# Performance work log

Hardware: AMD Instinct MI355X
Metric: run time of the kernel (lower is better)

Reference implementation:

```python
import jax, jax.numpy as jnp
import numpy as np

B, T, C = 48, 200, 53          # batch, timepoints, ICA components
E, H, A = 32, 64, 64            # embed dim, GRU hidden dim, attention hidden dim
C2 = C * C                      # 2809
E1 = round(0.05 * C2)           # gta_embed out = 140
E2 = round(0.5 * C2)            # gta_attend hidden = 1404
O = 2                           # output classes
BN_EPS = 1e-5


def setup_inputs() -> dict:
    key = jax.random.key(0)
    ks = jax.random.split(key, 24)
    n = lambda k, shape, s: jax.random.normal(k, shape, dtype=jnp.float32) * s
    return {
        "x": jax.random.normal(ks[0], (B, T, C), dtype=jnp.float32),
        "emb_w": n(ks[1], (E,), 0.3), "emb_b": n(ks[2], (E,), 0.1),
        "w_ih": n(ks[3], (3 * H, E), 0.12), "w_hh": n(ks[4], (3 * H, H), 0.12),
        "b_ih": n(ks[5], (3 * H,), 0.05), "b_hh": n(ks[6], (3 * H,), 0.05),
        "wq": n(ks[7], (A, H), 0.12), "bq": n(ks[8], (A,), 0.05),
        "wk": n(ks[9], (A, H), 0.12), "bk": n(ks[10], (A,), 0.05),
        "wv": n(ks[11], (H, H), 0.12), "bv": n(ks[12], (H,), 0.05),
        "u0": jax.random.normal(ks[13], (H,), dtype=jnp.float32),
        "w_g1": n(ks[14], (E1, C2), 0.02), "b_g1": n(ks[15], (E1,), 0.02),
        "bn_g": jnp.ones((E1,), jnp.float32), "bn_b": jnp.zeros((E1,), jnp.float32),
        "w_g2": n(ks[16], (E2, E1), 0.05), "b_g2": n(ks[17], (E2,), 0.05),
        "w_g3": n(ks[18], (1, E2), 0.02), "b_g3": n(ks[19], (1,), 0.02),
        "w_clf": n(ks[20], (O, C2), 0.02), "b_clf": jnp.zeros((O,), jnp.float32),
    }


def _normalize(v, eps=1e-12):
    return v / (jnp.linalg.norm(v) + eps)


def _gru_cell(x, h, w_ih, w_hh, b_ih, b_hh):
    # torch GRU cell math. x:(N,E) h:(N,H)
    gi = x @ w_ih.T + b_ih
    gh = h @ w_hh.T + b_hh
    i_r, i_z, i_n = jnp.split(gi, 3, axis=-1)
    h_r, h_z, h_n = jnp.split(gh, 3, axis=-1)
    r = jax.nn.sigmoid(i_r + h_r)
    z = jax.nn.sigmoid(i_z + h_z)
    n = jnp.tanh(i_n + r * h_n)
    return (1.0 - z) * n + z * h


def _forward(x, emb_w, emb_b, w_ih, w_hh, b_ih, b_hh, wq, bq, wk, bk, wv, bv, u0,
             w_g1, b_g1, bn_g, bn_b, w_g2, b_g2, w_g3, b_g3, w_clf, b_clf):
    Bs, Ts, Cs = x.shape
    Hd = wv.shape[0]
    # single shared Linear(1,E) embedding: (B,T,C) -> (T,B,C,E) for scan
    emb = x[..., None] * emb_w + emb_b
    emb = jnp.transpose(emb, (1, 0, 2, 3))
    h0 = jnp.zeros((Bs * Cs, Hd), x.dtype)

    def step(carry, emb_t):
        h, u = carry
        hg = _gru_cell(emb_t.reshape(Bs * Cs, -1), h, w_ih, w_hh, b_ih, b_hh)
        hb = hg.reshape(Bs, Cs, Hd)
        # spectral_norm on value weight: 5 power iterations (no_grad, as torch)
        v = None
        for _ in range(5):
            v = _normalize(wv.T @ u)
            u = _normalize(wv @ v)
        u = jax.lax.stop_gradient(u)
        v = jax.lax.stop_gradient(v)
        sigma = u @ (wv @ v)
        q = hb @ wq.T + bq          # (B,C,A)
        k = hb @ wk.T + bk          # (B,C,A)
        val = hb @ (wv / sigma).T + bv  # (B,C,H)
        scores = jnp.einsum('bia,bja->bij', q, k)  # (B,C,C)
        # eigenvalue-based spectral normalization (detached: track_grads=False)
        ev = jnp.linalg.eigvals(jax.lax.stop_gradient(scores))
        m = jnp.max(jnp.abs(ev), axis=1)[:, None, None].astype(x.dtype)
        attn = scores / m
        h_new = jnp.einsum('bij,bjh->bih', attn, val).reshape(Bs * Cs, Hd)
        return (h_new, u), attn

    (_, _), aligns = jax.lax.scan(step, (h0, u0), emb)  # aligns: (T,B,C,C)
    align = jnp.transpose(aligns, (1, 0, 2, 3))         # (B,T,C,C)
    Aflat = align.reshape(Bs, Ts, Cs * Cs)

    # gta_attention over the time axis
    xr = Aflat * Aflat.mean(axis=1, keepdims=True)
    flat = xr.reshape(Bs * Ts, Cs * Cs)
    e = flat @ w_g1.T + b_g1
    mu = e.mean(axis=0)
    var = e.var(axis=0)  # biased, as torch BatchNorm1d (training)
    e = jax.nn.relu((e - mu) / jnp.sqrt(var + BN_EPS) * bn_g + bn_b)
    a = jax.nn.relu(e @ w_g2.T + b_g2) @ w_g3.T + b_g3   # (B*T,1)
    a = jax.nn.softmax(a.reshape(Bs, Ts), axis=1)
    dnc = (Aflat * a[..., None]).sum(axis=1)             # (B,C*C)
    logits = dnc @ w_clf.T + b_clf
    return logits, dnc.reshape(Bs, Cs, Cs), align


def reference(x, emb_w, emb_b, w_ih, w_hh, b_ih, b_hh, wq, bq, wk, bk, wv, bv, u0,
              w_g1, b_g1, bn_g, bn_b, w_g2, b_g2, w_g3, b_g3, w_clf, b_clf):
    return _forward(x, emb_w, emb_b, w_ih, w_hh, b_ih, b_hh, wq, bq, wk, bk, wv, bv, u0,
                    w_g1, b_g1, bn_g, bn_b, w_g2, b_g2, w_g3, b_g3, w_clf, b_clf)
```

## Files before the change

kernel.cpp:

```cpp
#include <hip/hip_runtime.h>
#include <hip/hip_bf16.h>
#include <math.h>

#define B_  48
#define T_  200
#define C_  53
#define H_  64
#define C2_ 2809
#define E1_ 140
#define E2_ 1404
#define TS  60

typedef long long i64;

struct __align__(16) F4 { float v[4]; };

__device__ __forceinline__ float wredsum(float v){
  #pragma unroll
  for (int o = 32; o > 0; o >>= 1) v += __shfl_xor(v, o);
  return v;
}
__device__ __forceinline__ float sigm(float x){ return 1.f/(1.f + __expf(-x)); }
__device__ __forceinline__ float tanhx(float x){
  float a = fabsf(x);
  float e = __expf(-2.f*a);
  float t = (1.f - e)/(1.f + e);
  return copysignf(t, x);
}

__device__ __forceinline__ void eig_mm(const float* __restrict__ X, float* __restrict__ Y,
                                       int r0, int c0, float inv,
                                       float& essq, float& etrc){
  float ea0[4] = {0.f,0.f,0.f,0.f};
  float ea1[4] = {0.f,0.f,0.f,0.f};
  for (int kq = 0; kq < 13; kq++){
    int k4 = kq*4;
    F4 a0 = *(const F4*)&X[(r0+0)*TS + k4];
    F4 a1 = *(const F4*)&X[(r0+1)*TS + k4];
    F4 b0 = *(const F4*)&X[(k4+0)*TS + c0];
    F4 b1 = *(const F4*)&X[(k4+1)*TS + c0];
    F4 b2 = *(const F4*)&X[(k4+2)*TS + c0];
    F4 b3 = *(const F4*)&X[(k4+3)*TS + c0];
    #pragma unroll
    for (int ci = 0; ci < 4; ci++){
      ea0[ci] += a0.v[0]*b0.v[ci] + a0.v[1]*b1.v[ci] + a0.v[2]*b2.v[ci] + a0.v[3]*b3.v[ci];
      ea1[ci] += a1.v[0]*b0.v[ci] + a1.v[1]*b1.v[ci] + a1.v[2]*b2.v[ci] + a1.v[3]*b3.v[ci];
    }
  }
  {
    float a0 = X[(r0+0)*TS + 52], a1 = X[(r0+1)*TS + 52];
    F4 bb = *(const F4*)&X[52*TS + c0];
    #pragma unroll
    for (int ci = 0; ci < 4; ci++){ ea0[ci] += a0*bb.v[ci]; ea1[ci] += a1*bb.v[ci]; }
  }
  F4 o0, o1;
  #pragma unroll
  for (int ci = 0; ci < 4; ci++){
    o0.v[ci] = ea0[ci]*inv;
    o1.v[ci] = ea1[ci]*inv;
    essq += o0.v[ci]*o0.v[ci] + o1.v[ci]*o1.v[ci];
  }
  if (r0   >= c0 && r0   < c0+4) etrc += o0.v[r0-c0];
  if (r0+1 >= c0 && r0+1 < c0+4) etrc += o1.v[r0+1-c0];
  *(F4*)&Y[(r0+0)*TS + c0] = o0;
  *(F4*)&Y[(r0+1)*TS + c0] = o1;
}

#define OFF_SIGMA 0
#define OFF_WHHT  200
#define OFF_WZV   12488
#define OFF_WUV   20680
#define OFF_P     20812
#define OFF_R0    21004
#define OFF_MM    21196
#define OFF_M2    25292
#define OFF_M4    29388
#define OFF_M5    33484
#define OFF_AMEAN 37580
#define OFF_E     172412
#define OFF_CA    1516412
#define OFF_CB    1516552
#define OFF_APRE  1516692
#define OFF_A     1526292
#define OFF_G2T   1535892

__global__ void k_prep1(const float* __restrict__ w_hh, const float* __restrict__ wq,
                        const float* __restrict__ wk, const float* __restrict__ wv,
                        const float* __restrict__ w_ih, const float* __restrict__ emb_w,
                        const float* __restrict__ emb_b, const float* __restrict__ b_ih,
                        const float* __restrict__ bq, const float* __restrict__ bk,
                        const float* __restrict__ w_g2,
                        float* whhT, float* wzv, float* wuv, float* g2t,
                        float* p, float* r0){
  int idx0 = blockIdx.x*blockDim.x + threadIdx.x;
  int stride = gridDim.x*blockDim.x;
  for (int i = idx0; i < 64*192; i += stride){
    int kk = i/192, g = i%192;
    whhT[i] = w_hh[g*64 + kk];
  }
  for (int i = idx0; i < 8192; i += stride){
    int h = i >> 7, a = i & 127;
    if (a < 64){
      float g = 0.f;
      for (int m = 0; m < 64; m++) g += wq[m*64 + h]*wk[m*64 + a];
      wzv[i] = g;
    } else {
      wzv[i] = wv[(a-64)*64 + h];
    }
  }
  for (int i = idx0; i < 129; i += stride){
    if (i < 64){
      float s = 0.f;
      for (int m = 0; m < 64; m++) s += wq[m*64 + i]*bk[m];
      wuv[i] = s;
    } else if (i < 128){
      int h = i - 64;
      float s = 0.f;
      for (int m = 0; m < 64; m++) s += wk[m*64 + h]*bq[m];
      wuv[i] = s;
    } else {
      float s = 0.f;
      for (int m = 0; m < 64; m++) s += bq[m]*bk[m];
      wuv[128] = s;
    }
  }
  for (int i = idx0; i < 140*1404; i += stride){ int k = i/1404, n = i%1404; g2t[i] = w_g2[n*140+k]; }
  for (int i = idx0; i < 192; i += stride){
    float s1 = 0.f, s2 = 0.f;
    for (int e = 0; e < 32; e++){ float w = w_ih[i*32+e]; s1 += w*emb_w[e]; s2 += w*emb_b[e]; }
    p[i] = s1; r0[i] = s2 + b_ih[i];
  }
}

__global__ void k_prep2(const float* __restrict__ wv, const float* __restrict__ u0,
                        float* Wm, float* Wm2, float* Wm4, float* Wm5, float* sigma){
  int r = threadIdx.x;
  for (int c = 0; c < 64; c++){
    float s = 0.f;
    for (int k = 0; k < 64; k++) s += wv[r*64+k]*wv[c*64+k];
    Wm[r*64+c] = s;
  }
  __syncthreads();
  for (int c = 0; c < 64; c++){
    float s = 0.f;
    for (int k = 0; k < 64; k++) s += Wm[r*64+k]*Wm[k*64+c];
    Wm2[r*64+c] = s;
  }
  __syncthreads();
  for (int c = 0; c < 64; c++){
    float s = 0.f;
    for (int k = 0; k < 64; k++) s += Wm2[r*64+k]*Wm2[k*64+c];
    Wm4[r*64+c] = s;
  }
  __syncthreads();
  for (int c = 0; c < 64; c++){
    float s = 0.f;
    for (int k = 0; k < 64; k++) s += Wm4[r*64+k]*Wm[k*64+c];
    Wm5[r*64+c] = s;
  }
  __syncthreads();
  __shared__ float su[64];
  su[r] = u0[r];
  __syncthreads();
  for (int t = 0; t < T_; t++){
    float z = 0.f, w = 0.f;
    for (int k = 0; k < 64; k++){ float uk = su[k]; z += Wm4[r*64+k]*uk; w += Wm5[r*64+k]*uk; }
    float nw = wredsum(w*w);
    float zw = wredsum(z*w);
    float sg = sqrtf(nw / fmaxf(zw, 1e-35f));
    if (r == 0) sigma[t] = sg;
    float wn = w * (1.f/sqrtf(fmaxf(nw, 1e-35f)));
    __syncthreads();
    su[r] = wn;
    __syncthreads();
  }
}

__global__ __launch_bounds__(512, 1) void k_scan(
    const float* __restrict__ x, const float* __restrict__ b_hh,
    const float* __restrict__ bv,
    const float* __restrict__ whhT, const float* __restrict__ wzv,
    const float* __restrict__ wuv,
    const float* __restrict__ wp, const float* __restrict__ wr0,
    const float* __restrict__ sigma, float* __restrict__ outAL,
    float* __restrict__ wamean){
  __shared__ __align__(16) float L[34160];
  float* Lw  = L;
  float* Rh  = L + 12288;
  float* R4  = L + 16128;
  float* R3  = L + 19968;
  float* R2  = L + 23808;
  float* R1  = L + 27200;
  float* Lp  = L + 30560;
  float* Lr0 = L + 30752;
  float* Lbh = L + 30944;
  float* Lbv = L + 31136;
  float* Lrq = L + 31200;
  float* Lrk = L + 31256;
  float* Lsc = L + 31312;
  float* Lmean = L + 31344;
  int tid = threadIdx.x;
  int b = blockIdx.x;

  for (int i = tid; i < 3072; i += 512) *(F4*)&Lw[i*4] = *(const F4*)&whhT[i*4];
  for (int i = tid; i < 192; i += 512){ Lp[i] = wp[i]; Lr0[i] = wr0[i]; Lbh[i] = b_hh[i]; }
  for (int i = tid; i < 64; i += 512) Lbv[i] = bv[i];
  for (int i = tid; i < 18272; i += 512) L[12288 + i] = 0.f;
  for (int i = tid; i < 2816; i += 512) Lmean[i] = 0.f;
  __syncthreads();

  int ct4 = tid >> 4, jt4 = tid & 15;
  int c0g = ct4*4, j0g = jt4*4;
  int it14 = tid/14, jt14 = tid%14;
  int i0s = it14*4, j0s = jt14*4;
  int ctq = tid >> 5, gtq = tid & 31;
  int c0q = ctq*4, g0q = gtq*4;
  int erg = tid/14, ecg = tid%14;
  int er0 = erg*2, ec0 = ecg*4;

  const float c0v = wuv[128];

  for (int t = 0; t < T_; t++){
    if (tid < 32) Lsc[tid] = 0.f;
    if (tid < 224){
      float gacc[3][4][4];
      #pragma unroll
      for (int g = 0; g < 3; g++)
        #pragma unroll
        for (int ji = 0; ji < 4; ji++){
          float bb = Lbh[g*64 + j0g + ji];
          #pragma unroll
          for (int ci = 0; ci < 4; ci++) gacc[g][ji][ci] = bb;
        }
      for (int kk = 0; kk < 64; kk++){
        F4 hv = *(F4*)&Rh[kk*TS + c0g];
        F4 w0 = *(const F4*)&Lw[kk*192 + j0g];
        F4 w1 = *(const F4*)&Lw[kk*192 + 64 + j0g];
        F4 w2 = *(const F4*)&Lw[kk*192 + 128 + j0g];
        #pragma unroll
        for (int ji = 0; ji < 4; ji++)
          #pragma unroll
          for (int ci = 0; ci < 4; ci++){
            gacc[0][ji][ci] += hv.v[ci]*w0.v[ji];
            gacc[1][ji][ci] += hv.v[ci]*w1.v[ji];
            gacc[2][ji][ci] += hv.v[ci]*w2.v[ji];
          }
      }
      float xv[4];
      #pragma unroll
      for (int ci = 0; ci < 4; ci++){
        int c = c0g + ci;
        xv[ci] = (c < C_) ? x[(i64)(b*T_ + t)*C_ + c] : 0.f;
      }
      F4 p0 = *(F4*)&Lp[j0g], p1 = *(F4*)&Lp[64+j0g], p2 = *(F4*)&Lp[128+j0g];
      F4 q0 = *(F4*)&Lr0[j0g], q1 = *(F4*)&Lr0[64+j0g], q2 = *(F4*)&Lr0[128+j0g];
      #pragma unroll
      for (int ji = 0; ji < 4; ji++){
        F4 hold = *(F4*)&Rh[(j0g+ji)*TS + c0g];
        F4 o;
        #pragma unroll
        for (int ci = 0; ci < 4; ci++){
          float rr = sigm(xv[ci]*p0.v[ji] + q0.v[ji] + gacc[0][ji][ci]);
          float zz = sigm(xv[ci]*p1.v[ji] + q1.v[ji] + gacc[1][ji][ci]);
          float nn = tanhx(xv[ci]*p2.v[ji] + q2.v[ji] + rr*gacc[2][ji][ci]);
          float hg = (1.f - zz)*nn + zz*hold.v[ci];
          o.v[ci] = (c0g + ci < C_) ? hg : 0.f;
        }
        *(F4*)&R4[(j0g+ji)*TS + c0g] = o;
      }
    }
    __syncthreads();
    if (tid < 448){
      float acc[4][4];
      #pragma unroll
      for (int gi = 0; gi < 4; gi++)
        #pragma unroll
        for (int ci = 0; ci < 4; ci++) acc[gi][ci] = 0.f;
      for (int kk = 0; kk < 64; kk++){
        F4 a = *(F4*)&R4[kk*TS + c0q];
        F4 w = *(const F4*)&wzv[kk*128 + g0q];
        #pragma unroll
        for (int gi = 0; gi < 4; gi++)
          #pragma unroll
          for (int ci = 0; ci < 4; ci++) acc[gi][ci] += a.v[ci]*w.v[gi];
      }
      if (g0q < 64){
        #pragma unroll
        for (int gi = 0; gi < 4; gi++){
          F4 o;
          #pragma unroll
          for (int ci = 0; ci < 4; ci++) o.v[ci] = acc[gi][ci];
          *(F4*)&R3[(g0q+gi)*TS + c0q] = o;
        }
      } else {
        float invs = 1.f/sigma[t];
        int a0i = g0q - 64;
        #pragma unroll
        for (int ci = 0; ci < 4; ci++){
          int c = c0q + ci;
          if (c < C_){
            F4 o;
            #pragma unroll
            for (int gi = 0; gi < 4; gi++) o.v[gi] = acc[gi][ci]*invs + Lbv[a0i+gi];
            *(F4*)&R2[c*64 + a0i] = o;
          }
        }
      }
    } else if (tid < 504){
      int u = tid - 448;
      float rq = 0.f, rk = 0.f;
      if (u < C_){
        for (int h = 0; h < 64; h++){
          float hv = R4[h*TS + u];
          rq += hv*wuv[h];
          rk += hv*wuv[64+h];
        }
      }
      if (u < 56){ Lrq[u] = rq; Lrk[u] = rk; }
    }
    __syncthreads();
    {
      float sacc[4][4];
      float ssq = 0.f, trc = 0.f;
      if (tid < 196){
        #pragma unroll
        for (int ii = 0; ii < 4; ii++)
          #pragma unroll
          for (int jj = 0; jj < 4; jj++){
            int i = i0s + ii, j = j0s + jj;
            sacc[ii][jj] = (i < C_ && j < C_) ? (Lrq[i] + Lrk[j] + c0v) : 0.f;
          }
        for (int aq = 0; aq < 16; aq++){
          int a4 = aq*4;
          F4 qa0 = *(F4*)&R3[(a4+0)*TS + i0s];
          F4 qa1 = *(F4*)&R3[(a4+1)*TS + i0s];
          F4 qa2 = *(F4*)&R3[(a4+2)*TS + i0s];
          F4 qa3 = *(F4*)&R3[(a4+3)*TS + i0s];
          F4 kb0 = *(F4*)&R4[(a4+0)*TS + j0s];
          F4 kb1 = *(F4*)&R4[(a4+1)*TS + j0s];
          F4 kb2 = *(F4*)&R4[(a4+2)*TS + j0s];
          F4 kb3 = *(F4*)&R4[(a4+3)*TS + j0s];
          #pragma unroll
          for (int ii = 0; ii < 4; ii++)
            #pragma unroll
            for (int jj = 0; jj < 4; jj++)
              sacc[ii][jj] += qa0.v[ii]*kb0.v[jj] + qa1.v[ii]*kb1.v[jj]
                            + qa2.v[ii]*kb2.v[jj] + qa3.v[ii]*kb3.v[jj];
        }
        #pragma unroll
        for (int ii = 0; ii < 4; ii++){
          int i = i0s + ii;
          if (i < C_){
            F4 o;
            #pragma unroll
            for (int jj = 0; jj < 4; jj++){
              o.v[jj] = sacc[ii][jj];
              ssq += sacc[ii][jj]*sacc[ii][jj];
            }
            *(F4*)&R1[i*TS + j0s] = o;
            if (j0s <= i && i < j0s + 4) trc += sacc[ii][i - j0s];
          }
        }
      }
      ssq = wredsum(ssq); trc = wredsum(trc);
      if ((tid & 63) == 0){
        if (ssq != 0.f) atomicAdd(&Lsc[0], ssq);
        if (trc != 0.f) atomicAdd(&Lsc[1], trc);
      }
    }
    __syncthreads();
    {
      float inv0 = 1.f/fmaxf(Lsc[0], 1e-35f);
      float essq = 0.f, etrc = 0.f;
      if (tid < 378) eig_mm(R1, R3, er0, ec0, inv0, essq, etrc);
      essq = wredsum(essq); etrc = wredsum(etrc);
      if ((tid & 63) == 0){
        if (essq != 0.f) atomicAdd(&Lsc[2], essq);
        if (etrc != 0.f) atomicAdd(&Lsc[3], etrc);
      }
    }
    __syncthreads();
    float Gacc = 0.f, prevest = 1e30f, est = 0.f;
    int cnt = 0;
    float pssq = fmaxf(Lsc[0], 1e-35f), ptr1 = Lsc[1];
    float* Xb = R3; float* Yb = R4;
    for (int j = 2; j <= 13; j++){
      float sj = fmaxf(Lsc[2*(j-1)], 1e-35f);
      float tj = Lsc[2*(j-1)+1];
      int J = j - 2;
      float t1n = ptr1/sqrtf(pssq);
      float t2n = tj;
      float disc = 2.f*t2n - t1n*t1n;
      float rq = (disc >= 0.f) ? 0.5f*(fabsf(t1n) + sqrtf(disc))
                               : sqrtf(fmaxf(0.5f*(t1n*t1n - t2n), 1e-30f));
      rq = fminf(fmaxf(rq, 0.02f), 1.5f);
      est = Gacc + ldexpf(0.5f*log2f(pssq) + log2f(rq), -J);
      if (fabsf(est - prevest) < 1e-4f) cnt++; else cnt = 0;
      prevest = est;
      Gacc += ldexpf(log2f(pssq), -(J+1));
      if ((J >= 4 && cnt >= 1) || j == 13) break;
      pssq = sj; ptr1 = tj;
      {
        float inv = 1.f/sj;
        float essq = 0.f, etrc = 0.f;
        if (tid < 378) eig_mm(Xb, Yb, er0, ec0, inv, essq, etrc);
        essq = wredsum(essq); etrc = wredsum(etrc);
        if ((tid & 63) == 0){
          if (essq != 0.f) atomicAdd(&Lsc[2*j], essq);
          if (etrc != 0.f) atomicAdd(&Lsc[2*j+1], etrc);
        }
      }
      { float* tp = Xb; Xb = Yb; Yb = tp; }
      __syncthreads();
    }
    float invm = exp2f(-est);
    if (tid < 224){
      float hraw0[4] = {0.f,0.f,0.f,0.f};
      float hraw1[4] = {0.f,0.f,0.f,0.f};
      float hraw2[4] = {0.f,0.f,0.f,0.f};
      float hraw3[4] = {0.f,0.f,0.f,0.f};
      for (int kq = 0; kq < 13; kq++){
        int k4 = kq*4;
        F4 a0 = *(F4*)&R1[(c0g+0)*TS + k4];
        F4 a1 = *(F4*)&R1[(c0g+1)*TS + k4];
        F4 a2 = *(F4*)&R1[(c0g+2)*TS + k4];
        F4 a3 = *(F4*)&R1[(c0g+3)*TS + k4];
        F4 b0 = *(F4*)&R2[(k4+0)*64 + j0g];
        F4 b1 = *(F4*)&R2[(k4+1)*64 + j0g];
        F4 b2 = *(F4*)&R2[(k4+2)*64 + j0g];
        F4 b3 = *(F4*)&R2[(k4+3)*64 + j0g];
        #pragma unroll
        for (int jj = 0; jj < 4; jj++){
          hraw0[jj] += a0.v[0]*b0.v[jj] + a0.v[1]*b1.v[jj] + a0.v[2]*b2.v[jj] + a0.v[3]*b3.v[jj];
          hraw1[jj] += a1.v[0]*b0.v[jj] + a1.v[1]*b1.v[jj] + a1.v[2]*b2.v[jj] + a1.v[3]*b3.v[jj];
          hraw2[jj] += a2.v[0]*b0.v[jj] + a2.v[1]*b1.v[jj] + a2.v[2]*b2.v[jj] + a2.v[3]*b3.v[jj];
          hraw3[jj] += a3.v[0]*b0.v[jj] + a3.v[1]*b1.v[jj] + a3.v[2]*b2.v[jj] + a3.v[3]*b3.v[jj];
        }
      }
      {
        const int k = 52;
        float a0 = R1[(c0g+0)*TS + k], a1 = R1[(c0g+1)*TS + k];
        float a2 = R1[(c0g+2)*TS + k], a3 = R1[(c0g+3)*TS + k];
        F4 bb = *(F4*)&R2[k*64 + j0g];
        #pragma unroll
        for (int jj = 0; jj < 4; jj++){
          hraw0[jj] += a0*bb.v[jj];
          hraw1[jj] += a1*bb.v[jj];
          hraw2[jj] += a2*bb.v[jj];
          hraw3[jj] += a3*bb.v[jj];
        }
      }
      #pragma unroll
      for (int jj = 0; jj < 4; jj++){
        F4 o;
        o.v[0] = (c0g + 0 < C_) ? hraw0[jj]*invm : 0.f;
        o.v[1] = (c0g + 1 < C_) ? hraw1[jj]*invm : 0.f;
        o.v[2] = (c0g + 2 < C_) ? hraw2[jj]*invm : 0.f;
        o.v[3] = (c0g + 3 < C_) ? hraw3[jj]*invm : 0.f;
        *(F4*)&Rh[(j0g+jj)*TS + c0g] = o;
      }
    } else if (tid < 420){
      int u = tid - 224;
      int i0 = (u/14)*4, j0 = (u%14)*4;
      float* ALrow = outAL + (i64)(b*T_ + t)*C2_;
      #pragma unroll
      for (int ii = 0; ii < 4; ii++){
        int i = i0 + ii;
        if (i < C_){
          F4 s = *(F4*)&R1[i*TS + j0];
          #pragma unroll
          for (int jj = 0; jj < 4; jj++){
            int jc = j0 + jj;
            if (jc < C_){
              float v = s.v[jj]*invm;
              ALrow[i*C_ + jc] = v;
              Lmean[i*C_ + jc] += v;
            }
          }
        }
      }
    }
    __syncthreads();
  }
  for (int i = tid; i < C2_; i += 512)
    wamean[(i64)b*C2_ + i] = Lmean[i]*(1.f/(float)T_);
}

__global__ __launch_bounds__(128) void k_gemm1(const float* __restrict__ AL,
                                               const float* __restrict__ amean,
                                               const float* __restrict__ w_g1,
                                               float* __restrict__ e){
  __shared__ __align__(16) float At[64][68];
  __shared__ __align__(16) float Bt[64][148];
  int mt = blockIdx.x >> 2, ks = blockIdx.x & 3;
  int tid = threadIdx.x;
  float acc[8][12];
  #pragma unroll
  for (int ri = 0; ri < 8; ri++)
    #pragma unroll
    for (int ci = 0; ci < 12; ci++) acc[ri][ci] = 0.f;
  int rg = tid/12, cg = tid%12;
  int r0 = rg*8, cc0 = cg*12;
  for (int kb = 0; kb < 11; kb++){
    int k0 = (ks*11 + kb)*64;
    for (int idx = tid; idx < 4096; idx += 128){
      int r = idx >> 6, i = idx & 63;
      int kk = k0 + i;
      int row = mt*64 + r, bb = row/T_;
      float v = 0.f;
      if (kk < C2_) v = AL[(i64)row*C2_ + kk]*amean[(i64)bb*C2_ + kk];
      At[i][r] = v;
    }
    for (int idx = tid; idx < 9216; idx += 128){
      int c = idx >> 6, i = idx & 63;
      int kk = k0 + i;
      float v = 0.f;
      if (c < E1_ && kk < C2_) v = w_g1[(i64)c*C2_ + kk];
      Bt[i][c] = v;
    }
    __syncthreads();
    if (tid < 96){
      for (int i = 0; i < 64; i++){
        F4 a0 = *(F4*)&At[i][r0]; F4 a1 = *(F4*)&At[i][r0+4];
        F4 b0 = *(F4*)&Bt[i][cc0]; F4 b1 = *(F4*)&Bt[i][cc0+4]; F4 b2 = *(F4*)&Bt[i][cc0+8];
        #pragma unroll
        for (int ri = 0; ri < 8; ri++){
          float av = (ri < 4) ? a0.v[ri] : a1.v[ri-4];
          #pragma unroll
          for (int ci = 0; ci < 12; ci++){
            float bv = (ci < 4) ? b0.v[ci] : (ci < 8) ? b1.v[ci-4] : b2.v[ci-8];
            acc[ri][ci] += av*bv;
          }
        }
      }
    }
    __syncthreads();
  }
  if (tid < 96){
    #pragma unroll
    for (int ri = 0; ri < 8; ri++)
      #pragma unroll
      for (int ci = 0; ci < 12; ci++){
        int c = cc0 + ci;
        if (c < E1_) atomicAdd(&e[(i64)(mt*64 + r0 + ri)*E1_ + c], acc[ri][ci]);
      }
  }
}

__global__ void k_bnstats(const float* __restrict__ e, const float* __restrict__ bn_g,
                          const float* __restrict__ bn_b, float* cA, float* cB){
  __shared__ float s1a[256], s2a[256];
  int c = blockIdx.x, tid = threadIdx.x;
  float s1 = 0.f, s2 = 0.f;
  for (int row = tid; row < B_*T_; row += 256){
    float v = e[(i64)row*E1_ + c];
    s1 += v; s2 += v*v;
  }
  s1a[tid] = s1; s2a[tid] = s2; __syncthreads();
  for (int s = 128; s > 0; s >>= 1){
    if (tid < s){ s1a[tid] += s1a[tid+s]; s2a[tid] += s2a[tid+s]; }
    __syncthreads();
  }
  if (tid == 0){
    float n = (float)(B_*T_);
    float mu = s1a[0]/n;
    float var = s2a[0]/n - mu*mu;
    float a = bn_g[c]/sqrtf(var + 1e-5f);
    cA[c] = a; cB[c] = bn_b[c] - mu*a;
  }
}

__global__ __launch_bounds__(128) void k_gemm2(const float* __restrict__ e,
                                               const float* __restrict__ cA, const float* __restrict__ cB,
                                               const float* __restrict__ g2t,
                                               const float* __restrict__ b_g2, const float* __restrict__ w_g3,
                                               float* __restrict__ apre){
  __shared__ __align__(16) float At2[140][68];
  int mt = blockIdx.x/30, nc = blockIdx.x%30;
  int tid = threadIdx.x;
  int nbase = nc*48;
  for (int idx = tid; idx < 64*140; idx += 128){
    int r = idx/140, k = idx - r*140;
    float v = e[(i64)(mt*64 + r)*E1_ + k]*cA[k] + cB[k];
    At2[k][r] = fmaxf(v, 0.f);
  }
  __syncthreads();
  if (tid < 96){
    int rg = tid/6, ng = tid%6;
    int r0 = rg*4, n0 = nbase + ng*8;
    float acc[4][8];
    #pragma unroll
    for (int ri = 0; ri < 4; ri++)
      #pragma unroll
      for (int ni = 0; ni < 8; ni++) acc[ri][ni] = 0.f;
    for (int k = 0; k < E1_; k++){
      F4 a = *(F4*)&At2[k][r0];
      float bvv[8];
      if (n0 + 8 <= E2_){
        F4 b0 = *(const F4*)&g2t[(i64)k*E2_ + n0];
        F4 b1 = *(const F4*)&g2t[(i64)k*E2_ + n0 + 4];
        #pragma unroll
        for (int u = 0; u < 4; u++){ bvv[u] = b0.v[u]; bvv[u+4] = b1.v[u]; }
      } else {
        #pragma unroll
        for (int ni = 0; ni < 8; ni++){ int n = n0+ni; bvv[ni] = (n < E2_) ? g2t[(i64)k*E2_ + n] : 0.f; }
      }
      #pragma unroll
      for (int ri = 0; ri < 4; ri++)
        #pragma unroll
        for (int ni = 0; ni < 8; ni++) acc[ri][ni] += a.v[ri]*bvv[ni];
    }
    #pragma unroll
    for (int ri = 0; ri < 4; ri++){
      float s = 0.f;
      #pragma unroll
      for (int ni = 0; ni < 8; ni++){
        int n = n0 + ni;
        if (n < E2_){
          float a2 = acc[ri][ni] + b_g2[n];
          if (a2 > 0.f) s += a2*w_g3[n];
        }
      }
      atomicAdd(&apre[mt*64 + r0 + ri], s);
    }
  }
}

__global__ void k_soft(const float* __restrict__ apre, const float* __restrict__ b_clf,
                       float* __restrict__ wa, float* __restrict__ out){
  __shared__ float sr[256];
  int b = blockIdx.x, tid = threadIdx.x;
  float v = (tid < T_) ? apre[b*T_ + tid] : -3.4e38f;
  sr[tid] = v; __syncthreads();
  for (int s = 128; s > 0; s >>= 1){ if (tid < s) sr[tid] = fmaxf(sr[tid], sr[tid+s]); __syncthreads(); }
  float mx = sr[0]; __syncthreads();
  float ev = (tid < T_) ? __expf(v - mx) : 0.f;
  sr[tid] = ev; __syncthreads();
  for (int s = 128; s > 0; s >>= 1){ if (tid < s) sr[tid] += sr[tid+s]; __syncthreads(); }
  float den = sr[0];
  if (tid < T_) wa[b*T_ + tid] = ev/den;
  if (b == 0 && tid < 2*B_) out[tid] = b_clf[tid & 1];
}

__global__ void k_dnc(const float* __restrict__ AL, const float* __restrict__ wa,
                      const float* __restrict__ w_clf, float* __restrict__ out){
  int b = blockIdx.x/11, ch = blockIdx.x%11;
  int c2 = ch*256 + threadIdx.x;
  float acc = 0.f;
  if (c2 < C2_){
    for (int t = 0; t < T_; t++)
      acc += AL[(i64)(b*T_ + t)*C2_ + c2]*wa[b*T_ + t];
    out[96 + (i64)b*C2_ + c2] = acc;
  }
  float p0 = (c2 < C2_) ? acc*w_clf[c2]        : 0.f;
  float p1 = (c2 < C2_) ? acc*w_clf[C2_ + c2]  : 0.f;
  p0 = wredsum(p0); p1 = wredsum(p1);
  if ((threadIdx.x & 63) == 0){
    atomicAdd(&out[b*2 + 0], p0);
    atomicAdd(&out[b*2 + 1], p1);
  }
}

extern "C" void kernel_launch(void* const* d_in, const int* in_sizes, int n_in,
                              void* d_out, int out_size, void* d_ws, size_t ws_size,
                              hipStream_t stream){
  const float* x     = (const float*)d_in[0];
  const float* emb_w = (const float*)d_in[1];
  const float* emb_b = (const float*)d_in[2];
  const float* w_ih  = (const float*)d_in[3];
  const float* w_hh  = (const float*)d_in[4];
  const float* b_ih  = (const float*)d_in[5];
  const float* b_hh  = (const float*)d_in[6];
  const float* wq    = (const float*)d_in[7];
  const float* bq    = (const float*)d_in[8];
  const float* wk    = (const float*)d_in[9];
  const float* bk    = (const float*)d_in[10];
  const float* wv_in = (const float*)d_in[11];
  const float* bv    = (const float*)d_in[12];
  const float* u0    = (const float*)d_in[13];
  const float* w_g1  = (const float*)d_in[14];
  const float* bn_g  = (const float*)d_in[16];
  const float* bn_b  = (const float*)d_in[17];
  const float* w_g2  = (const float*)d_in[18];
  const float* b_g2  = (const float*)d_in[19];
  const float* w_g3  = (const float*)d_in[20];
  const float* w_clf = (const float*)d_in[22];
  const float* b_clf = (const float*)d_in[23];
  float* out = (float*)d_out;
  float* W = (float*)d_ws;

  float* wsig   = W + OFF_SIGMA;
  float* whhT   = W + OFF_WHHT;
  float* wzv    = W + OFF_WZV;
  float* wuv    = W + OFF_WUV;
  float* wp     = W + OFF_P;
  float* wr0    = W + OFF_R0;
  float* wM     = W + OFF_MM;
  float* wM2    = W + OFF_M2;
  float* wM4    = W + OFF_M4;
  float* wM5    = W + OFF_M5;
  float* wamean = W + OFF_AMEAN;
  float* we     = W + OFF_E;
  float* wcA    = W + OFF_CA;
  float* wcB    = W + OFF_CB;
  float* wapre  = W + OFF_APRE;
  float* wa     = W + OFF_A;
  float* wg2t   = W + OFF_G2T;

  float* outAL = out + 96 + (i64)B_*C2_;

  hipMemsetAsync(we, 0, (size_t)(B_*T_)*E1_*sizeof(float), stream);
  hipMemsetAsync(wapre, 0, (size_t)(B_*T_)*sizeof(float), stream);

  k_prep1<<<96, 256, 0, stream>>>(w_hh, wq, wk, wv_in, w_ih, emb_w, emb_b, b_ih, bq, bk,
                                  w_g2, whhT, wzv, wuv, wg2t, wp, wr0);
  k_prep2<<<1, 64, 0, stream>>>(wv_in, u0, wM, wM2, wM4, wM5, wsig);
  k_scan<<<B_, 512, 0, stream>>>(x, b_hh, bv, whhT, wzv, wuv, wp, wr0, wsig, outAL, wamean);
  k_gemm1<<<600, 128, 0, stream>>>(outAL, wamean, w_g1, we);
  k_bnstats<<<E1_, 256, 0, stream>>>(we, bn_g, bn_b, wcA, wcB);
  k_gemm2<<<150*30, 128, 0, stream>>>(we, wcA, wcB, wg2t, b_g2, w_g3, wapre);
  k_soft<<<B_, 256, 0, stream>>>(wapre, b_clf, wa, out);
  k_dnc<<<B_*11, 256, 0, stream>>>(outAL, wa, w_clf, out);
}
```

Before: 10.25 ms.

## Overlap GRU hidden-state and gate matmuls with eigen iterations in the scan

Measured after the change: 13.91 ms. +35.8%, slower.

```diff
diff --git a/kernel.cpp b/kernel.cpp
--- a/kernel.cpp
+++ b/kernel.cpp
@@ -66,6 +66,52 @@
   *(F4*)&Y[(r0+1)*TS + c0] = o1;
 }
 
+__device__ __forceinline__ void eig_mm3(const float* __restrict__ X, float* __restrict__ Y,
+                                        int r0, int c0, float inv,
+                                        float& essq, float& etrc){
+  float ea0[4] = {0.f,0.f,0.f,0.f};
+  float ea1[4] = {0.f,0.f,0.f,0.f};
+  float ea2[4] = {0.f,0.f,0.f,0.f};
+  for (int kq = 0; kq < 13; kq++){
+    int k4 = kq*4;
+    F4 a0 = *(const F4*)&X[(r0+0)*TS + k4];
+    F4 a1 = *(const F4*)&X[(r0+1)*TS + k4];
+    F4 a2 = *(const F4*)&X[(r0+2)*TS + k4];
+    F4 b0 = *(const F4*)&X[(k4+0)*TS + c0];
+    F4 b1 = *(const F4*)&X[(k4+1)*TS + c0];
+    F4 b2 = *(const F4*)&X[(k4+2)*TS + c0];
+    F4 b3 = *(const F4*)&X[(k4+3)*TS + c0];
+    #pragma unroll
+    for (int ci = 0; ci < 4; ci++){
+      ea0[ci] += a0.v[0]*b0.v[ci] + a0.v[1]*b1.v[ci] + a0.v[2]*b2.v[ci] + a0.v[3]*b3.v[ci];
+      ea1[ci] += a1.v[0]*b0.v[ci] + a1.v[1]*b1.v[ci] + a1.v[2]*b2.v[ci] + a1.v[3]*b3.v[ci];
+      ea2[ci] += a2.v[0]*b0.v[ci] + a2.v[1]*b1.v[ci] + a2.v[2]*b2.v[ci] + a2.v[3]*b3.v[ci];
+    }
+  }
+  {
+    float a0 = X[(r0+0)*TS + 52], a1 = X[(r0+1)*TS + 52], a2 = X[(r0+2)*TS + 52];
+    F4 bb = *(const F4*)&X[52*TS + c0];
+    #pragma unroll
+    for (int ci = 0; ci < 4; ci++){
+      ea0[ci] += a0*bb.v[ci]; ea1[ci] += a1*bb.v[ci]; ea2[ci] += a2*bb.v[ci];
+    }
+  }
+  F4 o0, o1, o2;
+  #pragma unroll
+  for (int ci = 0; ci < 4; ci++){
+    o0.v[ci] = ea0[ci]*inv;
+    o1.v[ci] = ea1[ci]*inv;
+    o2.v[ci] = ea2[ci]*inv;
+    essq += o0.v[ci]*o0.v[ci] + o1.v[ci]*o1.v[ci] + o2.v[ci]*o2.v[ci];
+  }
+  if (r0   >= c0 && r0   < c0+4) etrc += o0.v[r0-c0];
+  if (r0+1 >= c0 && r0+1 < c0+4) etrc += o1.v[r0+1-c0];
+  if (r0+2 >= c0 && r0+2 < c0+4) etrc += o2.v[r0+2-c0];
+  *(F4*)&Y[(r0+0)*TS + c0] = o0;
+  *(F4*)&Y[(r0+1)*TS + c0] = o1;
+  *(F4*)&Y[(r0+2)*TS + c0] = o2;
+}
+
 #define OFF_SIGMA 0
 #define OFF_WHHT  200
 #define OFF_WZV   12488
@@ -184,29 +230,27 @@
     const float* __restrict__ wp, const float* __restrict__ wr0,
     const float* __restrict__ sigma, float* __restrict__ outAL,
     float* __restrict__ wamean){
-  __shared__ __align__(16) float L[34160];
-  float* Lw  = L;
-  float* Rh  = L + 12288;
-  float* R4  = L + 16128;
-  float* R3  = L + 19968;
-  float* R2  = L + 23808;
-  float* R1  = L + 27200;
-  float* Lp  = L + 30560;
-  float* Lr0 = L + 30752;
-  float* Lbh = L + 30944;
-  float* Lbv = L + 31136;
-  float* Lrq = L + 31200;
-  float* Lrk = L + 31256;
-  float* Lsc = L + 31312;
-  float* Lmean = L + 31344;
+  __shared__ __align__(16) float L[32624];
+  float* Rh  = L;
+  float* R4  = L + 3840;
+  float* R3  = L + 7680;
+  float* R2  = L + 11520;
+  float* R1  = L + 14912;
+  float* Gb  = L + 18272;
+  float* Lmean = L + 29024;
+  float* Lp  = L + 31840;
+  float* Lr0 = L + 32032;
+  float* Lbh = L + 32224;
+  float* Lbv = L + 32416;
+  float* Lrq = L + 32480;
+  float* Lrk = L + 32536;
+  float* Lsc = L + 32592;
   int tid = threadIdx.x;
   int b = blockIdx.x;
 
-  for (int i = tid; i < 3072; i += 512) *(F4*)&Lw[i*4] = *(const F4*)&whhT[i*4];
+  for (int i = tid; i < 31840; i += 512) L[i] = 0.f;
   for (int i = tid; i < 192; i += 512){ Lp[i] = wp[i]; Lr0[i] = wr0[i]; Lbh[i] = b_hh[i]; }
   for (int i = tid; i < 64; i += 512) Lbv[i] = bv[i];
-  for (int i = tid; i < 18272; i += 512) L[12288 + i] = 0.f;
-  for (int i = tid; i < 2816; i += 512) Lmean[i] = 0.f;
   __syncthreads();
 
   int ct4 = tid >> 4, jt4 = tid & 15;
@@ -219,33 +263,11 @@
   int er0 = erg*2, ec0 = ecg*4;
 
   const float c0v = wuv[128];
+  float hinv = 1.0f;
 
   for (int t = 0; t < T_; t++){
     if (tid < 32) Lsc[tid] = 0.f;
     if (tid < 224){
-      float gacc[3][4][4];
-      #pragma unroll
-      for (int g = 0; g < 3; g++)
-        #pragma unroll
-        for (int ji = 0; ji < 4; ji++){
-          float bb = Lbh[g*64 + j0g + ji];
-          #pragma unroll
-          for (int ci = 0; ci < 4; ci++) gacc[g][ji][ci] = bb;
-        }
-      for (int kk = 0; kk < 64; kk++){
-        F4 hv = *(F4*)&Rh[kk*TS + c0g];
-        F4 w0 = *(const F4*)&Lw[kk*192 + j0g];
-        F4 w1 = *(const F4*)&Lw[kk*192 + 64 + j0g];
-        F4 w2 = *(const F4*)&Lw[kk*192 + 128 + j0g];
-        #pragma unroll
-        for (int ji = 0; ji < 4; ji++)
-          #pragma unroll
-          for (int ci = 0; ci < 4; ci++){
-            gacc[0][ji][ci] += hv.v[ci]*w0.v[ji];
-            gacc[1][ji][ci] += hv.v[ci]*w1.v[ji];
-            gacc[2][ji][ci] += hv.v[ci]*w2.v[ji];
-          }
-      }
       float xv[4];
       #pragma unroll
       for (int ci = 0; ci < 4; ci++){
@@ -256,17 +278,22 @@
       F4 q0 = *(F4*)&Lr0[j0g], q1 = *(F4*)&Lr0[64+j0g], q2 = *(F4*)&Lr0[128+j0g];
       #pragma unroll
       for (int ji = 0; ji < 4; ji++){
-        F4 hold = *(F4*)&Rh[(j0g+ji)*TS + c0g];
+        int jr = j0g + ji;
+        F4 g0 = *(F4*)&Gb[jr*56 + c0g];
+        F4 g1 = *(F4*)&Gb[(64+jr)*56 + c0g];
+        F4 g2 = *(F4*)&Gb[(128+jr)*56 + c0g];
+        F4 hr = *(F4*)&Rh[jr*TS + c0g];
+        float b0 = Lbh[jr], b1 = Lbh[64+jr], b2 = Lbh[128+jr];
         F4 o;
         #pragma unroll
         for (int ci = 0; ci < 4; ci++){
-          float rr = sigm(xv[ci]*p0.v[ji] + q0.v[ji] + gacc[0][ji][ci]);
-          float zz = sigm(xv[ci]*p1.v[ji] + q1.v[ji] + gacc[1][ji][ci]);
-          float nn = tanhx(xv[ci]*p2.v[ji] + q2.v[ji] + rr*gacc[2][ji][ci]);
-          float hg = (1.f - zz)*nn + zz*hold.v[ci];
+          float rr = sigm(xv[ci]*p0.v[ji] + q0.v[ji] + b0 + g0.v[ci]*hinv);
+          float zz = sigm(xv[ci]*p1.v[ji] + q1.v[ji] + b1 + g1.v[ci]*hinv);
+          float nn = tanhx(xv[ci]*p2.v[ji] + q2.v[ji] + rr*(b2 + g2.v[ci]*hinv));
+          float hg = (1.f - zz)*nn + zz*(hr.v[ci]*hinv);
           o.v[ci] = (c0g + ci < C_) ? hg : 0.f;
         }
-        *(F4*)&R4[(j0g+ji)*TS + c0g] = o;
+        *(F4*)&R4[jr*TS + c0g] = o;
       }
     }
     __syncthreads();
@@ -370,9 +397,59 @@
     }
     __syncthreads();
     {
-      float inv0 = 1.f/fmaxf(Lsc[0], 1e-35f);
       float essq = 0.f, etrc = 0.f;
-      if (tid < 378) eig_mm(R1, R3, er0, ec0, inv0, essq, etrc);
+      if (tid < 252){
+        float inv0 = 1.f/fmaxf(Lsc[0], 1e-35f);
+        int r0e = (tid/14)*3, c0e = (tid%14)*4;
+        eig_mm3(R1, R3, r0e, c0e, inv0, essq, etrc);
+      } else if (tid < 476){
+        int u = tid - 252;
+        int c0 = (u >> 4)*4, j0 = (u & 15)*4;
+        float hr0[4] = {0.f,0.f,0.f,0.f};
+        float hr1[4] = {0.f,0.f,0.f,0.f};
+        float hr2[4] = {0.f,0.f,0.f,0.f};
+        float hr3[4] = {0.f,0.f,0.f,0.f};
+        for (int kq = 0; kq < 13; kq++){
+          int k4 = kq*4;
+          F4 a0 = *(F4*)&R1[(c0+0)*TS + k4];
+          F4 a1 = *(F4*)&R1[(c0+1)*TS + k4];
+          F4 a2 = *(F4*)&R1[(c0+2)*TS + k4];
+          F4 a3 = *(F4*)&R1[(c0+3)*TS + k4];
+          F4 b0 = *(F4*)&R2[(k4+0)*64 + j0];
+          F4 b1 = *(F4*)&R2[(k4+1)*64 + j0];
+          F4 b2 = *(F4*)&R2[(k4+2)*64 + j0];
+          F4 b3 = *(F4*)&R2[(k4+3)*64 + j0];
+          #pragma unroll
+          for (int jj = 0; jj < 4; jj++){
+            hr0[jj] += a0.v[0]*b0.v[jj] + a0.v[1]*b1.v[jj] + a0.v[2]*b2.v[jj] + a0.v[3]*b3.v[jj];
+            hr1[jj] += a1.v[0]*b0.v[jj] + a1.v[1]*b1.v[jj] + a1.v[2]*b2.v[jj] + a1.v[3]*b3.v[jj];
+            hr2[jj] += a2.v[0]*b0.v[jj] + a2.v[1]*b1.v[jj] + a2.v[2]*b2.v[jj] + a2.v[3]*b3.v[jj];
+            hr3[jj] += a3.v[0]*b0.v[jj] + a3.v[1]*b1.v[jj] + a3.v[2]*b2.v[jj] + a3.v[3]*b3.v[jj];
+          }
+        }
+        {
+          const int k = 52;
+          float a0 = R1[(c0+0)*TS + k], a1 = R1[(c0+1)*TS + k];
+          float a2 = R1[(c0+2)*TS + k], a3 = R1[(c0+3)*TS + k];
+          F4 bb = *(F4*)&R2[k*64 + j0];
+          #pragma unroll
+          for (int jj = 0; jj < 4; jj++){
+            hr0[jj] += a0*bb.v[jj];
+            hr1[jj] += a1*bb.v[jj];
+            hr2[jj] += a2*bb.v[jj];
+            hr3[jj] += a3*bb.v[jj];
+          }
+        }
+        #pragma unroll
+        for (int jj = 0; jj < 4; jj++){
+          F4 o;
+          o.v[0] = (c0 + 0 < C_) ? hr0[jj] : 0.f;
+          o.v[1] = (c0 + 1 < C_) ? hr1[jj] : 0.f;
+          o.v[2] = (c0 + 2 < C_) ? hr2[jj] : 0.f;
+          o.v[3] = (c0 + 3 < C_) ? hr3[jj] : 0.f;
+          *(F4*)&Rh[(j0+jj)*TS + c0] = o;
+        }
+      }
       essq = wredsum(essq); etrc = wredsum(etrc);
       if ((tid & 63) == 0){
         if (essq != 0.f) atomicAdd(&Lsc[2], essq);
@@ -403,7 +480,39 @@
       {
         float inv = 1.f/sj;
         float essq = 0.f, etrc = 0.f;
-        if (tid < 378) eig_mm(Xb, Yb, er0, ec0, inv, essq, etrc);
+        if (tid < 378){
+          eig_mm(Xb, Yb, er0, ec0, inv, essq, etrc);
+        } else if (tid < 490 && J < 4){
+          int sp = tid - 378;
+          int g3 = J*48 + (sp/7)*3;
+          int c8 = (sp%7)*8;
+          float acc[3][8];
+          #pragma unroll
+          for (int gi = 0; gi < 3; gi++)
+            #pragma unroll
+            for (int ci = 0; ci < 8; ci++) acc[gi][ci] = 0.f;
+          for (int kk = 0; kk < 64; kk++){
+            float w0 = whhT[kk*192 + g3 + 0];
+            float w1 = whhT[kk*192 + g3 + 1];
+            float w2 = whhT[kk*192 + g3 + 2];
+            F4 h0 = *(F4*)&Rh[kk*TS + c8];
+            F4 h1 = *(F4*)&Rh[kk*TS + c8 + 4];
+            #pragma unroll
+            for (int ci = 0; ci < 4; ci++){
+              acc[0][ci] += h0.v[ci]*w0; acc[0][ci+4] += h1.v[ci]*w0;
+              acc[1][ci] += h0.v[ci]*w1; acc[1][ci+4] += h1.v[ci]*w1;
+              acc[2][ci] += h0.v[ci]*w2; acc[2][ci+4] += h1.v[ci]*w2;
+            }
+          }
+          #pragma unroll
+          for (int gi = 0; gi < 3; gi++){
+            F4 lo, hi;
+            #pragma unroll
+            for (int ci = 0; ci < 4; ci++){ lo.v[ci] = acc[gi][ci]; hi.v[ci] = acc[gi][ci+4]; }
+            *(F4*)&Gb[(g3+gi)*56 + c8] = lo;
+            *(F4*)&Gb[(g3+gi)*56 + c8 + 4] = hi;
+          }
+        }
         essq = wredsum(essq); etrc = wredsum(etrc);
         if ((tid & 63) == 0){
           if (essq != 0.f) atomicAdd(&Lsc[2*j], essq);
@@ -414,63 +523,17 @@
       __syncthreads();
     }
     float invm = exp2f(-est);
-    if (tid < 224){
-      float hraw0[4] = {0.f,0.f,0.f,0.f};
-      float hraw1[4] = {0.f,0.f,0.f,0.f};
-      float hraw2[4] = {0.f,0.f,0.f,0.f};
-      float hraw3[4] = {0.f,0.f,0.f,0.f};
-      for (int kq = 0; kq < 13; kq++){
-        int k4 = kq*4;
-        F4 a0 = *(F4*)&R1[(c0g+0)*TS + k4];
-        F4 a1 = *(F4*)&R1[(c0g+1)*TS + k4];
-        F4 a2 = *(F4*)&R1[(c0g+2)*TS + k4];
-        F4 a3 = *(F4*)&R1[(c0g+3)*TS + k4];
-        F4 b0 = *(F4*)&R2[(k4+0)*64 + j0g];
-        F4 b1 = *(F4*)&R2[(k4+1)*64 + j0g];
-        F4 b2 = *(F4*)&R2[(k4+2)*64 + j0g];
-        F4 b3 = *(F4*)&R2[(k4+3)*64 + j0g];
-        #pragma unroll
-        for (int jj = 0; jj < 4; jj++){
-          hraw0[jj] += a0.v[0]*b0.v[jj] + a0.v[1]*b1.v[jj] + a0.v[2]*b2.v[jj] + a0.v[3]*b3.v[jj];
-          hraw1[jj] += a1.v[0]*b0.v[jj] + a1.v[1]*b1.v[jj] + a1.v[2]*b2.v[jj] + a1.v[3]*b3.v[jj];
-          hraw2[jj] += a2.v[0]*b0.v[jj] + a2.v[1]*b1.v[jj] + a2.v[2]*b2.v[jj] + a2.v[3]*b3.v[jj];
-          hraw3[jj] += a3.v[0]*b0.v[jj] + a3.v[1]*b1.v[jj] + a3.v[2]*b2.v[jj] + a3.v[3]*b3.v[jj];
-        }
-      }
-      {
-        const int k = 52;
-        float a0 = R1[(c0g+0)*TS + k], a1 = R1[(c0g+1)*TS + k];
-        float a2 = R1[(c0g+2)*TS + k], a3 = R1[(c0g+3)*TS + k];
-        F4 bb = *(F4*)&R2[k*64 + j0g];
-        #pragma unroll
-        for (int jj = 0; jj < 4; jj++){
-          hraw0[jj] += a0*bb.v[jj];
-          hraw1[jj] += a1*bb.v[jj];
-          hraw2[jj] += a2*bb.v[jj];
-          hraw3[jj] += a3*bb.v[jj];
-        }
-      }
-      #pragma unroll
-      for (int jj = 0; jj < 4; jj++){
-        F4 o;
-        o.v[0] = (c0g + 0 < C_) ? hraw0[jj]*invm : 0.f;
-        o.v[1] = (c0g + 1 < C_) ? hraw1[jj]*invm : 0.f;
-        o.v[2] = (c0g + 2 < C_) ? hraw2[jj]*invm : 0.f;
-        o.v[3] = (c0g + 3 < C_) ? hraw3[jj]*invm : 0.f;
-        *(F4*)&Rh[(j0g+jj)*TS + c0g] = o;
-      }
-    } else if (tid < 420){
-      int u = tid - 224;
-      int i0 = (u/14)*4, j0 = (u%14)*4;
+    hinv = invm;
+    if (tid < 196){
       float* ALrow = outAL + (i64)(b*T_ + t)*C2_;
       #pragma unroll
       for (int ii = 0; ii < 4; ii++){
-        int i = i0 + ii;
+        int i = i0s + ii;
         if (i < C_){
-          F4 s = *(F4*)&R1[i*TS + j0];
+          F4 s = *(F4*)&R1[i*TS + j0s];
           #pragma unroll
           for (int jj = 0; jj < 4; jj++){
-            int jc = j0 + jj;
+            int jc = j0s + jj;
             if (jc < C_){
               float v = s.v[jj]*invm;
               ALrow[i*C_ + jc] = v;
```
